# Optimization experiments

Measured on AMD Instinct MI355X. Metric: run time of the kernel, lower is better.

## Reference

```python
import jax, jax.numpy as jnp
import numpy as np

DIM = 64
NUM_GRAPHS = 512


def setup_inputs() -> dict:
    key = jax.random.key(0)
    ks = jax.random.split(key, 24)
    N, E, F = 20000, 60000, 11
    rn = lambda k, s, sc: jax.random.normal(k, s, jnp.float32) * sc
    return {
        "x": jax.random.normal(ks[0], (N, F), jnp.float32),
        "edge_index": jax.random.randint(ks[1], (2, E), 0, N),
        "edge_attr": jax.random.uniform(ks[2], (E, 5), jnp.float32),
        "batch": jnp.sort(jax.random.randint(ks[3], (N,), 0, NUM_GRAPHS)),
        # lin0: num_features -> dim
        "lin0_w": rn(ks[4], (DIM, F), 0.3), "lin0_b": jnp.zeros(DIM, jnp.float32),
        # edge MLP: 5 -> 128 -> dim*dim
        "nn1_w": rn(ks[5], (128, 5), 0.3), "nn1_b": jnp.zeros(128, jnp.float32),
        "nn2_w": rn(ks[6], (DIM * DIM, 128), 0.02), "nn2_b": jnp.zeros(DIM * DIM, jnp.float32),
        # NNConv root weight + bias
        "root_w": rn(ks[7], (DIM, DIM), 0.1), "conv_b": jnp.zeros(DIM, jnp.float32),
        # GRU (input dim, hidden dim) gates r,z,n
        "gru_w_ih": rn(ks[8], (3 * DIM, DIM), 0.1), "gru_w_hh": rn(ks[9], (3 * DIM, DIM), 0.1),
        "gru_b_ih": jnp.zeros(3 * DIM, jnp.float32), "gru_b_hh": jnp.zeros(3 * DIM, jnp.float32),
        # Set2Set LSTM: input 2*dim, hidden dim, gates i,f,g,o
        "lstm_w_ih": rn(ks[10], (4 * DIM, 2 * DIM), 0.1), "lstm_w_hh": rn(ks[11], (4 * DIM, DIM), 0.1),
        "lstm_b_ih": jnp.zeros(4 * DIM, jnp.float32), "lstm_b_hh": jnp.zeros(4 * DIM, jnp.float32),
        # readout
        "lin1_w": rn(ks[12], (DIM, 2 * DIM), 0.1), "lin1_b": jnp.zeros(DIM, jnp.float32),
        "lin2_w": rn(ks[13], (1, DIM), 0.1), "lin2_b": jnp.zeros(1, jnp.float32),
    }


def reference(x, edge_index, edge_attr, batch,
              lin0_w, lin0_b, nn1_w, nn1_b, nn2_w, nn2_b, root_w, conv_b,
              gru_w_ih, gru_w_hh, gru_b_ih, gru_b_hh,
              lstm_w_ih, lstm_w_hh, lstm_b_ih, lstm_b_hh,
              lin1_w, lin1_b, lin2_w, lin2_b):
    N = x.shape[0]
    src, dst = edge_index[0], edge_index[1]
    # per-edge weight matrices from edge MLP (edge_attr is constant across the 3 conv calls)
    We = (jax.nn.relu(edge_attr @ nn1_w.T + nn1_b) @ nn2_w.T + nn2_b).reshape(-1, DIM, DIM)
    deg = jnp.maximum(jax.ops.segment_sum(jnp.ones_like(src, jnp.float32), dst, N), 1.0)[:, None]

    out = jax.nn.relu(x @ lin0_w.T + lin0_b)
    h = out  # GRU hidden, shape [N, dim]
    for _ in range(3):
        # NNConv: gather src -> per-edge matmul -> scatter-mean at dst, plus root + bias
        msg = jnp.einsum('ei,eio->eo', out[src], We)
        agg = jax.ops.segment_sum(msg, dst, N) / deg
        m = jax.nn.relu(agg + out @ root_w.T + conv_b)
        # single GRU step (PyTorch gate layout r,z,n)
        gi = m @ gru_w_ih.T + gru_b_ih
        gh = h @ gru_w_hh.T + gru_b_hh
        ir, iz, inn = jnp.split(gi, 3, -1)
        hr, hz, hn = jnp.split(gh, 3, -1)
        r = jax.nn.sigmoid(ir + hr)
        z = jax.nn.sigmoid(iz + hz)
        n = jnp.tanh(inn + r * hn)
        h = (1.0 - z) * n + z * h
        out = h

    # Set2Set pooling, 3 processing steps
    B = NUM_GRAPHS
    q_star = jnp.zeros((B, 2 * DIM), out.dtype)
    hs = jnp.zeros((B, DIM), out.dtype)
    cs = jnp.zeros((B, DIM), out.dtype)
    for _ in range(3):
        gates = q_star @ lstm_w_ih.T + lstm_b_ih + hs @ lstm_w_hh.T + lstm_b_hh
        gi, gf, gg, go = jnp.split(gates, 4, -1)
        cs = jax.nn.sigmoid(gf) * cs + jax.nn.sigmoid(gi) * jnp.tanh(gg)
        hs = jax.nn.sigmoid(go) * jnp.tanh(cs)
        q = hs
        e = jnp.sum(out * q[batch], axis=-1)                 # [N]
        emax = jax.ops.segment_max(e, batch, B)
        a = jnp.exp(e - emax[batch])
        a = a / jax.ops.segment_sum(a, batch, B)[batch]      # scatter-softmax
        r_ = jax.ops.segment_sum(a[:, None] * out, batch, B)  # [B, dim]
        q_star = jnp.concatenate([q, r_], axis=-1)

    y = jax.nn.relu(q_star @ lin1_w.T + lin1_b) @ lin2_w.T + lin2_b
    return y.reshape(-1)
```

## Files before the change

kernel.cpp:

```cpp
#include <hip/hip_runtime.h>
#include <math.h>


typedef _Float16 f16x8 __attribute__((ext_vector_type(8)));
typedef _Float16 h2 __attribute__((ext_vector_type(2)));
typedef float f32x4 __attribute__((ext_vector_type(4)));

#define BFRAG_TOTAL (66 * 4 * 4 * 64 * 8)
#define PAIRS_CAP 40064
#define PMAX 152
#define SPLITK 4
#define ITERS 8

#if __has_builtin(__builtin_amdgcn_fdot2)
#define FDOT2(a, b, c) __builtin_amdgcn_fdot2((a), (b), (c), false)
#else
__device__ __forceinline__ float FDOT2(h2 a, h2 b, float c) {
  return c + (float)a[0] * (float)b[0] + (float)a[1] * (float)b[1];
}
#endif

__global__ void k_gptr(const int* __restrict__ batch, int* __restrict__ gptr,
                       int N, int B) {
  int n = blockIdx.x * 256 + threadIdx.x;
  if (n >= N) return;
  int b = batch[n];
  int bp = (n == 0) ? -1 : batch[n - 1];
  for (int g = bp + 1; g <= b; ++g) gptr[g] = n;
  if (n == N - 1) {
    for (int g = b + 1; g <= B; ++g) gptr[g] = N;
  }
}

__global__ void k_cnt(const int* __restrict__ eidx, int* __restrict__ cnt, int E) {
  int e = blockIdx.x * 256 + threadIdx.x;
  if (e < E) atomicAdd(&cnt[eidx[E + e]], 1);
}

__global__ __launch_bounds__(1024) void k_scan(const int* __restrict__ cnt,
                                               int* __restrict__ dptr2, int N) {
  __shared__ int wsum[16];
  int t = threadIdx.x;
  int lane = t & 63, wid = t >> 6;
  if (t == 0) dptr2[0] = 0;
  int running = 0;
  for (int base = 0; base < N; base += 1024) {
    int x = (base + t < N) ? ((cnt[base + t] + 1) & ~1) : 0;
#pragma unroll
    for (int d = 1; d < 64; d <<= 1) {
      int u = __shfl_up(x, d, 64);
      if (lane >= d) x += u;
    }
    if (lane == 63) wsum[wid] = x;
    __syncthreads();
    if (wid == 0) {
      int y = (lane < 16) ? wsum[lane] : 0;
#pragma unroll
      for (int d = 1; d < 16; d <<= 1) {
        int u = __shfl_up(y, d, 64);
        if (lane >= d) y += u;
      }
      if (lane < 16) wsum[lane] = y;
    }
    __syncthreads();
    int add = running + (wid > 0 ? wsum[wid - 1] : 0);
    if (base + t < N) dptr2[base + t + 1] = add + x;
    running += wsum[15];
    __syncthreads();
  }
}

__global__ void k_fill(const int* __restrict__ eidx, const int* __restrict__ dptr2,
                       int* __restrict__ fill, int* __restrict__ srcs_s,
                       int* __restrict__ eord, int E) {
  int e = blockIdx.x * 256 + threadIdx.x;
  if (e >= E) return;
  int d = eidx[E + e];
  int pos = dptr2[d] + atomicAdd(&fill[d], 1);
  srcs_s[pos] = eidx[e];
  eord[pos] = e;
}

__global__ __launch_bounds__(256) void k_h1t(const float* __restrict__ eattr,
                                             const int* __restrict__ eord,
                                             const int* __restrict__ eidx,
                                             const int* __restrict__ cnt,
                                             const float* __restrict__ nn1_w,
                                             const float* __restrict__ nn1_b,
                                             f16x8* __restrict__ hp, int E) {
  __shared__ float w5[640];
  __shared__ float bb[128];
  __shared__ float at[128][10];
  __shared__ float idg[128];
  __shared__ float vf1[128];
  const int t = threadIdx.x;
  const int m0 = blockIdx.x * 128;
  for (int idx = t; idx < 640; idx += 256) w5[idx] = nn1_w[idx];
  if (t < 128) bb[t] = nn1_b[t];
  if (t < 128) {
    int m = m0 + t;
    int e0 = eord[2 * m], e1 = eord[2 * m + 1];
    float iv = 0.f, vf = 0.f;
    if (e0 >= 0) {
      const float* a = eattr + (size_t)e0 * 5;
#pragma unroll
      for (int q = 0; q < 5; ++q) at[t][q] = a[q];
      int dg = cnt[eidx[E + e0]];
      iv = 1.f / (float)(dg > 1 ? dg : 1);
      if (e1 >= 0) {
        const float* b = eattr + (size_t)e1 * 5;
#pragma unroll
        for (int q = 0; q < 5; ++q) at[t][5 + q] = b[q];
        vf = 1.f;
      } else {
#pragma unroll
        for (int q = 0; q < 5; ++q) at[t][5 + q] = 0.f;
      }
    } else {
#pragma unroll
      for (int q = 0; q < 10; ++q) at[t][q] = 0.f;
    }
    idg[t] = iv;
    vf1[t] = vf;
  }
  __syncthreads();
  const int pl = t & 127, jh = (t >> 7) * 64;
  const int m = m0 + pl;
  float a0 = at[pl][0], a1 = at[pl][1], a2 = at[pl][2], a3 = at[pl][3],
        a4 = at[pl][4];
  float b0 = at[pl][5], b1 = at[pl][6], b2 = at[pl][7], b3 = at[pl][8],
        b4 = at[pl][9];
  float iv = idg[pl], vf = vf1[pl];
#pragma unroll 4
  for (int ci = 0; ci < 16; ++ci) {
    int j0 = jh + ci * 4;
    f16x8 o;
#pragma unroll
    for (int u = 0; u < 4; ++u) {
      const float* wr = &w5[(j0 + u) * 5];
      float v0 = fmaxf(bb[j0 + u] + a0 * wr[0] + a1 * wr[1] + a2 * wr[2] +
                           a3 * wr[3] + a4 * wr[4], 0.f) * iv;
      float v1 = fmaxf(bb[j0 + u] + b0 * wr[0] + b1 * wr[1] + b2 * wr[2] +
                           b3 * wr[3] + b4 * wr[4], 0.f) * iv * vf;
      o[2 * u] = (_Float16)v0;
      o[2 * u + 1] = (_Float16)v1;
    }
    hp[(size_t)(j0 >> 2) * PAIRS_CAP + m] = o;
  }
}

__global__ __launch_bounds__(256) void k_bsplit(
    const float* __restrict__ nn2_w, const float* __restrict__ nn2_b,
    const float* __restrict__ root_w, _Float16* __restrict__ Bh,
    _Float16* __restrict__ Bl) {
  __shared__ float lds[4096 * 2];
  const int kc = blockIdx.x;
  const int t = threadIdx.x;
  if (kc < 64) {
    for (int r = t; r < 4096; r += 256) {
      float2 v = *(const float2*)&nn2_w[(size_t)r * 128 + kc * 2];
      lds[r * 2] = v.x;
      lds[r * 2 + 1] = v.y;
    }
  } else if (kc == 64) {
    for (int r = t; r < 4096; r += 256) {
      lds[r * 2] = nn2_b[r];
      lds[r * 2 + 1] = 0.f;
    }
  } else {
    for (int r = t; r < 4096; r += 256) {
      int i = r >> 6, o = r & 63;
      lds[r * 2] = root_w[o * 64 + i];
      lds[r * 2 + 1] = 0.f;
    }
  }
  __syncthreads();
  for (int slot = t; slot < 1024; slot += 256) {
    int lane = slot & 63, c = (slot >> 6) & 3, w = slot >> 8;
    f16x8 ph, pl;
#pragma unroll
    for (int j = 0; j < 8; ++j) {
      int mm = w * 32 + ((lane >> 4) << 3) + j;
      int o = c * 16 + (lane & 15);
      int i = mm & 63, kl = mm >> 6;
      float v = lds[(i * 64 + o) * 2 + kl];
      _Float16 h = (_Float16)v;
      ph[j] = h;
      pl[j] = (_Float16)(v - (float)h);
    }
    size_t base = (((size_t)kc * 4 + w) * 4 + c) * 512 + (size_t)lane * 8;
    *(f16x8*)&Bh[base] = ph;
    *(f16x8*)&Bl[base] = pl;
  }
}

__global__ void k_lin0(const float* __restrict__ x, const float* __restrict__ w,
                       const float* __restrict__ b, float* __restrict__ outn, int N) {
  int gid = blockIdx.x * 256 + threadIdx.x;
  int n = gid >> 6, d = gid & 63;
  if (n >= N) return;
  const float* xr = x + (size_t)n * 11;
  const float* wr = w + d * 11;
  float acc = b[d];
#pragma unroll
  for (int f = 0; f < 11; ++f) acc += xr[f] * wr[f];
  outn[(size_t)n * 64 + d] = fmaxf(acc, 0.f);
}

__global__ __launch_bounds__(512, 4) void k_fused(
    const float* __restrict__ outn, const f16x8* __restrict__ hp,
    const int* __restrict__ dptr2, const int* __restrict__ cnt,
    const int* __restrict__ srcs_s, const _Float16* __restrict__ Bh,
    const _Float16* __restrict__ Bl, float* __restrict__ agg2, int N) {
  __shared__ __align__(16) _Float16 Ah[32 * 64 * 8];
  __shared__ uint4 sbufq[PMAX * 17];
  __shared__ uint4 hpq[2][PMAX];

  const int t = threadIdx.x;
  const int w = t >> 6, lane = t & 63;
  const int wq = w & 3;
  const int c_off = (w >> 2) * 2;
  const int nl = t >> 3;
  const int io = t & 7;
  const int split = blockIdx.y;
  const int n0 = blockIdx.x * 64;
  const int n = n0 + nl;
  const bool nvalid = (n < N);
  const int hi_n = (n0 + 64 > N) ? N : (n0 + 64);
  const int p0b = dptr2[n0];
  const int p1b = dptr2[hi_n];
  const int MP0 = p0b >> 1;
  const int MPn = (p1b - p0b) >> 1;
  const bool useLds = (MPn <= PMAX);
  int mp0 = 0, mp1 = 0, deg = 0;
  if (nvalid) { mp0 = dptr2[n] >> 1; mp1 = dptr2[n + 1] >> 1; deg = cnt[n]; }
  const float inv = 1.f / (float)(deg > 1 ? deg : 1);
  const int odd = deg & 1;
  const int rt_b = nl >> 4, nm = nl & 15;
  const int MPs = useLds ? MPn : 0;

  for (int idx = t; idx < MPs * 16; idx += 512) {
    int ml = idx >> 4, g = idx & 15;
    int e0s = srcs_s[2 * (MP0 + ml)];
    int e1s = srcs_s[2 * (MP0 + ml) + 1];
    float4 r0 = *(const float4*)(outn + (size_t)e0s * 64 + g * 4);
    float4 r1 = *(const float4*)(outn + (size_t)e1s * 64 + g * 4);
    f16x8 o;
    o[0] = (_Float16)r0.x; o[1] = (_Float16)r1.x;
    o[2] = (_Float16)r0.y; o[3] = (_Float16)r1.y;
    o[4] = (_Float16)r0.z; o[5] = (_Float16)r1.z;
    o[6] = (_Float16)r0.w; o[7] = (_Float16)r1.w;
    sbufq[ml * 17 + (((g >> 2) ^ (ml & 3)) << 2) + (g & 3)] =
        __builtin_bit_cast(uint4, o);
  }
  for (int idx = t; idx < MPs; idx += 512)
    hpq[0][idx] =
        *(const uint4*)&hp[(size_t)(split * ITERS) * PAIRS_CAP + MP0 + idx];
  __syncthreads();

  f32x4 acc[4][2];
#pragma unroll
  for (int a = 0; a < 4; ++a)
#pragma unroll
    for (int c = 0; c < 2; ++c) acc[a][c] = (f32x4)(0.f);

  const int niter = (split == 0) ? (ITERS + 1) : ITERS;
  int cur = 0;
  for (int cc = 0; cc < niter; ++cc) {
    const bool extra = (cc == ITERS);

    float av[4][8];
#pragma unroll
    for (int kl = 0; kl < 4; ++kl)
#pragma unroll
      for (int j = 0; j < 8; ++j) av[kl][j] = 0.f;

    if (!extra) {
      if (useLds) {
        for (int m = mp0; m < mp1; ++m) {
          int ml = m - MP0;
          uint4 hu = hpq[cur][ml];
          h2 h0 = __builtin_bit_cast(h2, hu.x);
          h2 h1 = __builtin_bit_cast(h2, hu.y);
          h2 hh2 = __builtin_bit_cast(h2, hu.z);
          h2 h3 = __builtin_bit_cast(h2, hu.w);
          int sb = ml * 17 + (((io >> 1) ^ (ml & 3)) << 2) + (io & 1) * 2;
          uint4 su0 = sbufq[sb], su1 = sbufq[sb + 1];
          unsigned vs[8] = {su0.x, su0.y, su0.z, su0.w,
                            su1.x, su1.y, su1.z, su1.w};
#pragma unroll
          for (int v = 0; v < 8; ++v) {
            h2 sp = __builtin_bit_cast(h2, vs[v]);
            av[0][v] = FDOT2(h0, sp, av[0][v]);
            av[1][v] = FDOT2(h1, sp, av[1][v]);
            av[2][v] = FDOT2(hh2, sp, av[2][v]);
            av[3][v] = FDOT2(h3, sp, av[3][v]);
          }
        }
      } else {
        const f16x8* hc = hp + (size_t)(split * ITERS + cc) * PAIRS_CAP;
        for (int m = mp0; m < mp1; ++m) {
          f16x8 hv = hc[m];
          int e0s = srcs_s[2 * m], e1s = srcs_s[2 * m + 1];
          const float4* pa = (const float4*)(outn + (size_t)e0s * 64 + io * 8);
          const float4* pb = (const float4*)(outn + (size_t)e1s * 64 + io * 8);
          float4 a0 = pa[0], a1 = pa[1];
          float4 c0 = pb[0], c1 = pb[1];
          float sv0[8] = {a0.x, a0.y, a0.z, a0.w, a1.x, a1.y, a1.z, a1.w};
          float sv1[8] = {c0.x, c0.y, c0.z, c0.w, c1.x, c1.y, c1.z, c1.w};
#pragma unroll
          for (int kl = 0; kl < 4; ++kl) {
            float hA = (float)hv[2 * kl], hB = (float)hv[2 * kl + 1];
#pragma unroll
            for (int j = 0; j < 8; ++j)
              av[kl][j] += hA * sv0[j] + hB * sv1[j];
          }
        }
      }
    } else {
      if (useLds) {
        for (int m = mp0; m < mp1; ++m) {
          int ml = m - MP0;
          h2 msk;
          msk[0] = (_Float16)1.f;
          msk[1] = (_Float16)((odd && m == mp1 - 1) ? 0.f : 1.f);
          int sb = ml * 17 + (((io >> 1) ^ (ml & 3)) << 2) + (io & 1) * 2;
          uint4 su0 = sbufq[sb], su1 = sbufq[sb + 1];
          unsigned vs[8] = {su0.x, su0.y, su0.z, su0.w,
                            su1.x, su1.y, su1.z, su1.w};
#pragma unroll
          for (int v = 0; v < 8; ++v) {
            h2 sp = __builtin_bit_cast(h2, vs[v]);
            av[0][v] = FDOT2(msk, sp, av[0][v]);
          }
        }
      } else {
        for (int m = mp0; m < mp1; ++m) {
          float m1 = (odd && m == mp1 - 1) ? 0.f : 1.f;
          int e0s = srcs_s[2 * m], e1s = srcs_s[2 * m + 1];
          const float4* pa = (const float4*)(outn + (size_t)e0s * 64 + io * 8);
          const float4* pb = (const float4*)(outn + (size_t)e1s * 64 + io * 8);
          float4 a0 = pa[0], a1 = pa[1];
          float4 c0 = pb[0], c1 = pb[1];
          float sv0[8] = {a0.x, a0.y, a0.z, a0.w, a1.x, a1.y, a1.z, a1.w};
          float sv1[8] = {c0.x, c0.y, c0.z, c0.w, c1.x, c1.y, c1.z, c1.w};
#pragma unroll
          for (int j = 0; j < 8; ++j) av[0][j] += sv0[j] + m1 * sv1[j];
        }
      }
#pragma unroll
      for (int j = 0; j < 8; ++j) av[0][j] *= inv;
      if (nvalid) {
        const float4* sp = (const float4*)(outn + (size_t)n * 64 + io * 8);
        float4 s0 = sp[0], s1 = sp[1];
        float sv[8] = {s0.x, s0.y, s0.z, s0.w, s1.x, s1.y, s1.z, s1.w};
#pragma unroll
        for (int j = 0; j < 8; ++j) av[2][j] = sv[j];
      }
    }

#pragma unroll
    for (int kl = 0; kl < 4; ++kl) {
      const int wb = (kl & 1) * 2 + (io >> 2);
      const int q = ((io >> 1) & 1) * 2 + (io & 1);
      const int fb = (kl >> 1) * 16 + wb * 4 + rt_b;
      const int base = (fb * 64 + (q << 4) + nm) * 8;
      f16x8 phv;
#pragma unroll
      for (int jj = 0; jj < 8; ++jj) phv[jj] = (_Float16)av[kl][jj];
      *(f16x8*)&Ah[base] = phv;
    }
    __syncthreads();

#pragma unroll
    for (int ph = 0; ph < 2; ++ph) {
      const int kco = extra ? (64 + ph) : (split * 16 + cc * 2 + ph);
      f16x8 ah[4];
#pragma unroll
      for (int rt = 0; rt < 4; ++rt)
        ah[rt] = *(const f16x8*)&Ah[((ph * 16 + wq * 4 + rt) * 64 + lane) * 8];
      if (ph == 0 && t < 256 && cc + 1 < ITERS) {
        const uint4* hc =
            (const uint4*)&hp[(size_t)(split * ITERS + cc + 1) * PAIRS_CAP + MP0];
        for (int idx = t; idx < MPs; idx += 256) hpq[cur ^ 1][idx] = hc[idx];
      }
      size_t bbase = ((size_t)(kco * 4 + wq) * 4) * 512;
#pragma unroll
      for (int c2 = 0; c2 < 2; ++c2) {
        const int c = c_off + c2;
        f16x8 bh = *(const f16x8*)&Bh[bbase + c * 512 + lane * 8];
        f16x8 bl = *(const f16x8*)&Bl[bbase + c * 512 + lane * 8];
#pragma unroll
        for (int rt = 0; rt < 4; ++rt) {
          acc[rt][c2] = __builtin_amdgcn_mfma_f32_16x16x32_f16(ah[rt], bh, acc[rt][c2], 0, 0, 0);
          acc[rt][c2] = __builtin_amdgcn_mfma_f32_16x16x32_f16(ah[rt], bl, acc[rt][c2], 0, 0, 0);
        }
      }
    }
    __syncthreads();
    if (cc + 1 < ITERS) cur ^= 1;
  }

  {
    float* redb = (float*)Ah;
    const int qrow = (lane >> 4) * 4, col15 = lane & 15;
    const int g14 = ((lane >> 4) & 1) << 4;
    if (wq == 1 || wq == 3) {
      float* L = redb + (wq >> 1) * 4096;
#pragma unroll
      for (int rt = 0; rt < 4; ++rt)
#pragma unroll
        for (int r = 0; r < 4; ++r) {
          int row = rt * 16 + qrow + r;
#pragma unroll
          for (int c2 = 0; c2 < 2; ++c2) {
            int col = (c_off + c2) * 16 + col15;
            L[row * 64 + (col ^ g14)] = acc[rt][c2][r];
          }
        }
    }
    __syncthreads();
    if (wq == 0 || wq == 2) {
      const float* L = redb + (wq >> 1) * 4096;
#pragma unroll
      for (int rt = 0; rt < 4; ++rt)
#pragma unroll
        for (int r = 0; r < 4; ++r) {
          int row = rt * 16 + qrow + r;
#pragma unroll
          for (int c2 = 0; c2 < 2; ++c2) {
            int col = (c_off + c2) * 16 + col15;
            acc[rt][c2][r] += L[row * 64 + (col ^ g14)];
          }
        }
    }
    __syncthreads();
    if (wq == 2) {
      float* L = redb;
#pragma unroll
      for (int rt = 0; rt < 4; ++rt)
#pragma unroll
        for (int r = 0; r < 4; ++r) {
          int row = rt * 16 + qrow + r;
#pragma unroll
          for (int c2 = 0; c2 < 2; ++c2) {
            int col = (c_off + c2) * 16 + col15;
            L[row * 64 + (col ^ g14)] = acc[rt][c2][r];
          }
        }
    }
    __syncthreads();
    if (wq == 0) {
      const float* L = redb;
      float* ag = agg2 + (size_t)split * (size_t)N * 64;
#pragma unroll
      for (int rt = 0; rt < 4; ++rt)
#pragma unroll
        for (int r = 0; r < 4; ++r) {
          int row = rt * 16 + qrow + r;
          int nn = n0 + row;
          if (nn < N) {
#pragma unroll
            for (int c2 = 0; c2 < 2; ++c2) {
              int col = (c_off + c2) * 16 + col15;
              float v = acc[rt][c2][r] + L[row * 64 + (col ^ g14)];
              ag[(size_t)nn * 64 + col] = v;
            }
          }
        }
    }
  }
}

__global__ __launch_bounds__(256) void k_gru(
    const float* __restrict__ agg2, const float* __restrict__ conv_b,
    const float* __restrict__ gw_ih, const float* __restrict__ gw_hh,
    const float* __restrict__ gb_ih, const float* __restrict__ gb_hh,
    float* __restrict__ outn, int N) {
  __shared__ float wT[32 * 385];
  const int t = threadIdx.x;
  const int wv = t >> 6, d = t & 63;
  const int nbase = blockIdx.x * 16 + wv * 4;
  const size_t NN = (size_t)N * 64;
  float m_d[4], h_d[4];
  bool act[4];
#pragma unroll
  for (int j = 0; j < 4; ++j) {
    int n = nbase + j;
    act[j] = (n < N);
    if (act[j]) {
      size_t idx = (size_t)n * 64 + d;
      float s = agg2[idx] + agg2[NN + idx] + agg2[2 * NN + idx] +
                agg2[3 * NN + idx];
      m_d[j] = fmaxf(s + conv_b[d], 0.f);
      h_d[j] = outn[idx];
    } else {
      m_d[j] = 0.f;
      h_d[j] = 0.f;
    }
  }
  float ir[4] = {0, 0, 0, 0}, iz[4] = {0, 0, 0, 0}, in_[4] = {0, 0, 0, 0};
  float hr[4] = {0, 0, 0, 0}, hz[4] = {0, 0, 0, 0}, hn[4] = {0, 0, 0, 0};
  for (int half = 0; half < 2; ++half) {
    __syncthreads();
    for (int idx = t; idx < 192 * 32; idx += 256) {
      int g = idx >> 5, kl = idx & 31;
      wT[kl * 385 + g] = gw_ih[g * 64 + half * 32 + kl];
      wT[kl * 385 + 192 + g] = gw_hh[g * 64 + half * 32 + kl];
    }
    __syncthreads();
#pragma unroll
    for (int kl = 0; kl < 32; ++kl) {
      int k = half * 32 + kl;
      const float* row = &wT[kl * 385];
      float r0 = row[d], r1 = row[64 + d], r2 = row[128 + d];
      float r3 = row[192 + d], r4 = row[256 + d], r5 = row[320 + d];
#pragma unroll
      for (int j = 0; j < 4; ++j) {
        float mk = __shfl(m_d[j], k);
        float hk = __shfl(h_d[j], k);
        ir[j] += r0 * mk;
        iz[j] += r1 * mk;
        in_[j] += r2 * mk;
        hr[j] += r3 * hk;
        hz[j] += r4 * hk;
        hn[j] += r5 * hk;
      }
    }
  }
#pragma unroll
  for (int j = 0; j < 4; ++j) {
    if (act[j]) {
      int n = nbase + j;
      float r = 1.f / (1.f + expf(-(ir[j] + gb_ih[d] + hr[j] + gb_hh[d])));
      float z = 1.f / (1.f + expf(-(iz[j] + gb_ih[64 + d] + hz[j] + gb_hh[64 + d])));
      float nn = tanhf(in_[j] + gb_ih[128 + d] + r * (hn[j] + gb_hh[128 + d]));
      outn[(size_t)n * 64 + d] = (1.f - z) * nn + z * h_d[j];
    }
  }
}

__global__ __launch_bounds__(256) void k_s2s(
    const float* __restrict__ outn, const int* __restrict__ gptr,
    const float* __restrict__ w_ih, const float* __restrict__ w_hh,
    const float* __restrict__ b_ih, const float* __restrict__ b_hh,
    const float* __restrict__ w1, const float* __restrict__ b1,
    const float* __restrict__ w2, const float* __restrict__ b2,
    float* __restrict__ y) {
  __shared__ float q[128];
  __shared__ float hsL[64];
  __shared__ float csL[64];
  __shared__ float gate[256];
  __shared__ float red[4][66];
  const int b = blockIdx.x, t = threadIdx.x;
  const int wv = t >> 6, d = t & 63;
  const int n0 = gptr[b], n1 = gptr[b + 1];
  if (t < 128) q[t] = 0.f;
  if (t < 64) { hsL[t] = 0.f; csL[t] = 0.f; }
  __syncthreads();

  for (int step = 0; step < 3; ++step) {
    float acc = b_ih[t] + b_hh[t];
    const float* wi = w_ih + t * 128;
    const float* wh = w_hh + t * 64;
#pragma unroll 4
    for (int k = 0; k < 128; ++k) acc += wi[k] * q[k];
#pragma unroll 4
    for (int k = 0; k < 64; ++k) acc += wh[k] * hsL[k];
    gate[t] = acc;
    __syncthreads();
    if (t < 64) {
      float ig = gate[t], fg = gate[64 + t], gg = gate[128 + t],
            og = gate[192 + t];
      float c = csL[t];
      float si = 1.f / (1.f + expf(-ig));
      float sf = 1.f / (1.f + expf(-fg));
      float so = 1.f / (1.f + expf(-og));
      float cn = sf * c + si * tanhf(gg);
      csL[t] = cn;
      hsL[t] = so * tanhf(cn);
    }
    __syncthreads();

    float qd = hsL[d];
    float mx = -3.4e38f, den = 0.f, racc = 0.f;
    for (int nn = n0 + wv; nn < n1; nn += 4) {
      float od = outn[(size_t)nn * 64 + d];
      float v = od * qd;
      for (int s = 32; s > 0; s >>= 1) v += __shfl_xor(v, s);
      float mnew = fmaxf(mx, v);
      float scale = expf(mx - mnew);
      float a = expf(v - mnew);
      den = den * scale + a;
      racc = racc * scale + a * od;
      mx = mnew;
    }
    if (d == 0) { red[wv][0] = mx; red[wv][1] = den; }
    red[wv][2 + d] = racc;
    __syncthreads();
    if (t < 64) {
      float M = fmaxf(fmaxf(red[0][0], red[1][0]), fmaxf(red[2][0], red[3][0]));
      float dd = 0.f, rr = 0.f;
#pragma unroll
      for (int ww = 0; ww < 4; ++ww) {
        float sc = expf(red[ww][0] - M);
        dd += red[ww][1] * sc;
        rr += red[ww][2 + t] * sc;
      }
      float r = (dd > 0.f) ? rr / dd : 0.f;
      q[t] = hsL[t];
      q[64 + t] = r;
    }
    __syncthreads();
  }

  if (t < 64) {
    float acc = b1[t];
    const float* wr = w1 + t * 128;
#pragma unroll 4
    for (int k = 0; k < 128; ++k) acc += wr[k] * q[k];
    acc = fmaxf(acc, 0.f) * w2[t];
    for (int s = 32; s > 0; s >>= 1) acc += __shfl_xor(acc, s);
    if (t == 0) y[b] = acc + b2[0];
  }
}

extern "C" void kernel_launch(void* const* d_in, const int* in_sizes, int n_in,
                              void* d_out, int out_size, void* d_ws,
                              size_t ws_size, hipStream_t stream) {
  (void)n_in; (void)out_size; (void)ws_size;
  const float* x      = (const float*)d_in[0];
  const int*   eidx   = (const int*)d_in[1];
  const float* eattr  = (const float*)d_in[2];
  const int*   batch  = (const int*)d_in[3];
  const float* lin0_w = (const float*)d_in[4];
  const float* lin0_b = (const float*)d_in[5];
  const float* nn1_w  = (const float*)d_in[6];
  const float* nn1_b  = (const float*)d_in[7];
  const float* nn2_w  = (const float*)d_in[8];
  const float* nn2_b  = (const float*)d_in[9];
  const float* root_w = (const float*)d_in[10];
  const float* conv_b = (const float*)d_in[11];
  const float* gw_ih  = (const float*)d_in[12];
  const float* gw_hh  = (const float*)d_in[13];
  const float* gb_ih  = (const float*)d_in[14];
  const float* gb_hh  = (const float*)d_in[15];
  const float* lw_ih  = (const float*)d_in[16];
  const float* lw_hh  = (const float*)d_in[17];
  const float* lb_ih  = (const float*)d_in[18];
  const float* lb_hh  = (const float*)d_in[19];
  const float* lin1_w = (const float*)d_in[20];
  const float* lin1_b = (const float*)d_in[21];
  const float* lin2_w = (const float*)d_in[22];
  const float* lin2_b = (const float*)d_in[23];

  const int N = in_sizes[0] / 11;
  const int E = in_sizes[1] / 2;
  const int B = 512;

  size_t off = 0;
  auto bump = [&](size_t bytes) {
    size_t o = off;
    off += (bytes + 255) & ~(size_t)255;
    return o;
  };
  char* base = (char*)d_ws;
  float*     outn   = (float*)(base + bump((size_t)N * 64 * 4));
  float*     agg2   = (float*)(base + bump((size_t)SPLITK * N * 64 * 4));
  f16x8*     hpG    = (f16x8*)(base + bump((size_t)32 * PAIRS_CAP * 16));
  _Float16*  Bh     = (_Float16*)(base + bump((size_t)BFRAG_TOTAL * 2));
  _Float16*  Bl     = (_Float16*)(base + bump((size_t)BFRAG_TOTAL * 2));
  int*       cnt    = (int*)(base + bump((size_t)2 * N * 4));
  int*       fill   = cnt + N;
  int*       dptr2  = (int*)(base + bump((size_t)(N + 1) * 4));
  int*       srcs_s = (int*)(base + bump((size_t)2 * PAIRS_CAP * 4));
  int*       eord   = (int*)(base + bump((size_t)2 * PAIRS_CAP * 4));
  int*       gptr   = (int*)(base + bump((size_t)(B + 1) * 4));

  hipMemsetAsync(cnt, 0, (size_t)2 * N * 4, stream);
  hipMemsetAsync(srcs_s, 0, (size_t)2 * PAIRS_CAP * 4, stream);
  hipMemsetAsync(eord, 0xFF, (size_t)2 * PAIRS_CAP * 4, stream);

  k_gptr<<<(N + 255) / 256, 256, 0, stream>>>(batch, gptr, N, B);
  k_cnt<<<(E + 255) / 256, 256, 0, stream>>>(eidx, cnt, E);
  k_scan<<<1, 1024, 0, stream>>>(cnt, dptr2, N);
  k_fill<<<(E + 255) / 256, 256, 0, stream>>>(eidx, dptr2, fill, srcs_s, eord, E);
  k_h1t<<<PAIRS_CAP / 128, 256, 0, stream>>>(eattr, eord, eidx, cnt, nn1_w,
                                             nn1_b, hpG, E);
  k_bsplit<<<66, 256, 0, stream>>>(nn2_w, nn2_b, root_w, Bh, Bl);
  k_lin0<<<(N * 64 + 255) / 256, 256, 0, stream>>>(x, lin0_w, lin0_b, outn, N);

  const int NBLK = (N + 63) / 64;
  for (int it = 0; it < 3; ++it) {
    k_fused<<<dim3(NBLK, SPLITK), 512, 0, stream>>>(outn, hpG, dptr2, cnt,
                                                    srcs_s, Bh, Bl, agg2, N);
    k_gru<<<(N + 15) / 16, 256, 0, stream>>>(agg2, conv_b, gw_ih, gw_hh, gb_ih,
                                             gb_hh, outn, N);
  }

  k_s2s<<<B, 256, 0, stream>>>(outn, gptr, lw_ih, lw_hh, lb_ih, lb_hh, lin1_w,
                               lin1_b, lin2_w, lin2_b, (float*)d_out);
}
```

Before: 715.9 us.

## Move GRU gate matmuls onto MFMA with split-fp16 pre-packed weights

Replaces the scalar FMA/shuffle GRU kernel with one that stages the [m|h] activations as fp16 A-fragments in LDS. It computes the r, z and n gate products with 16x16x32 f16 MFMAs against weights pre-split into high and low fp16 halves by a new one-time packing kernel. The goal is to cut the FP32 ALU cost and the per-block weight transpose into LDS that each GRU launch repeated. In exchange, activations are rounded to a single fp16, which loses precision, and the bias and gate math now sit in the MFMA output layout.

```diff
diff --git a/kernel.cpp b/kernel.cpp
--- a/kernel.cpp
+++ b/kernel.cpp
@@ -7,6 +7,7 @@
 typedef float f32x4 __attribute__((ext_vector_type(4)));
 
 #define BFRAG_TOTAL (66 * 4 * 4 * 64 * 8)
+#define GFRAG_TOTAL (4 * 16 * 64 * 8)
 #define PAIRS_CAP 40064
 #define PMAX 152
 #define SPLITK 4
@@ -194,6 +195,38 @@
   }
 }
 
+__global__ __launch_bounds__(256) void k_gsplit(
+    const float* __restrict__ gw_ih, const float* __restrict__ gw_hh,
+    _Float16* __restrict__ Gh, _Float16* __restrict__ Gl) {
+  const int c = blockIdx.x;
+  const int t = threadIdx.x;
+  const int w = t >> 6, lane = t & 63;
+  const int part = c >> 2, dblk = c & 3;
+  f16x8 oh, ol;
+#pragma unroll
+  for (int j = 0; j < 8; ++j) {
+    int k = w * 32 + ((lane >> 4) << 3) + j;
+    int d = dblk * 16 + (lane & 15);
+    float v;
+    if (part == 0) {
+      v = (k < 64) ? gw_ih[(size_t)d * 64 + k] : gw_hh[(size_t)d * 64 + (k - 64)];
+    } else if (part == 1) {
+      v = (k < 64) ? gw_ih[(size_t)(64 + d) * 64 + k]
+                   : gw_hh[(size_t)(64 + d) * 64 + (k - 64)];
+    } else if (part == 2) {
+      v = (k < 64) ? gw_ih[(size_t)(128 + d) * 64 + k] : 0.f;
+    } else {
+      v = (k >= 64) ? gw_hh[(size_t)(128 + d) * 64 + (k - 64)] : 0.f;
+    }
+    _Float16 h = (_Float16)v;
+    oh[j] = h;
+    ol[j] = (_Float16)(v - (float)h);
+  }
+  size_t base = ((size_t)(w * 16 + c) * 64 + lane) * 8;
+  *(f16x8*)&Gh[base] = oh;
+  *(f16x8*)&Gl[base] = ol;
+}
+
 __global__ void k_lin0(const float* __restrict__ x, const float* __restrict__ w,
                        const float* __restrict__ b, float* __restrict__ outn, int N) {
   int gid = blockIdx.x * 256 + threadIdx.x;
@@ -472,70 +505,99 @@
   }
 }
 
-__global__ __launch_bounds__(256) void k_gru(
+__global__ __launch_bounds__(512) void k_gru2(
     const float* __restrict__ agg2, const float* __restrict__ conv_b,
-    const float* __restrict__ gw_ih, const float* __restrict__ gw_hh,
+    const _Float16* __restrict__ Gh, const _Float16* __restrict__ Gl,
     const float* __restrict__ gb_ih, const float* __restrict__ gb_hh,
     float* __restrict__ outn, int N) {
-  __shared__ float wT[32 * 385];
+  __shared__ __align__(16) _Float16 Afrag[16 * 64 * 8];
+  __shared__ float bih[192], bhh[192];
   const int t = threadIdx.x;
-  const int wv = t >> 6, d = t & 63;
-  const int nbase = blockIdx.x * 16 + wv * 4;
+  const int n0 = blockIdx.x * 64;
   const size_t NN = (size_t)N * 64;
-  float m_d[4], h_d[4];
-  bool act[4];
-#pragma unroll
-  for (int j = 0; j < 4; ++j) {
-    int n = nbase + j;
-    act[j] = (n < N);
-    if (act[j]) {
-      size_t idx = (size_t)n * 64 + d;
-      float s = agg2[idx] + agg2[NN + idx] + agg2[2 * NN + idx] +
-                agg2[3 * NN + idx];
-      m_d[j] = fmaxf(s + conv_b[d], 0.f);
-      h_d[j] = outn[idx];
+  if (t < 192) { bih[t] = gb_ih[t]; bhh[t] = gb_hh[t]; }
+
+  {
+    const int nl = t >> 3, io = t & 7;
+    const int n = n0 + nl;
+    float v[16];
+    if (n < N) {
+      if (io < 4) {
+        const int d0 = io * 16;
+        const size_t base = (size_t)n * 64 + d0;
+#pragma unroll
+        for (int q = 0; q < 4; ++q) {
+          float4 s0 = *(const float4*)&agg2[base + q * 4];
+          float4 s1 = *(const float4*)&agg2[NN + base + q * 4];
+          float4 s2 = *(const float4*)&agg2[2 * NN + base + q * 4];
+          float4 s3 = *(const float4*)&agg2[3 * NN + base + q * 4];
+          float4 cb = *(const float4*)&conv_b[d0 + q * 4];
+          v[q * 4 + 0] = fmaxf(s0.x + s1.x + s2.x + s3.x + cb.x, 0.f);
+          v[q * 4 + 1] = fmaxf(s0.y + s1.y + s2.y + s3.y + cb.y, 0.f);
+          v[q * 4 + 2] = fmaxf(s0.z + s1.z + s2.z + s3.z + cb.z, 0.f);
+          v[q * 4 + 3] = fmaxf(s0.w + s1.w + s2.w + s3.w + cb.w, 0.f);
+        }
+      } else {
+        const int d0 = (io - 4) * 16;
+#pragma unroll
+        for (int q = 0; q < 4; ++q) {
+          float4 h4 = *(const float4*)&outn[(size_t)n * 64 + d0 + q * 4];
+          v[q * 4 + 0] = h4.x;
+          v[q * 4 + 1] = h4.y;
+          v[q * 4 + 2] = h4.z;
+          v[q * 4 + 3] = h4.w;
+        }
+      }
     } else {
-      m_d[j] = 0.f;
-      h_d[j] = 0.f;
-    }
-  }
-  float ir[4] = {0, 0, 0, 0}, iz[4] = {0, 0, 0, 0}, in_[4] = {0, 0, 0, 0};
-  float hr[4] = {0, 0, 0, 0}, hz[4] = {0, 0, 0, 0}, hn[4] = {0, 0, 0, 0};
-  for (int half = 0; half < 2; ++half) {
-    __syncthreads();
-    for (int idx = t; idx < 192 * 32; idx += 256) {
-      int g = idx >> 5, kl = idx & 31;
-      wT[kl * 385 + g] = gw_ih[g * 64 + half * 32 + kl];
-      wT[kl * 385 + 192 + g] = gw_hh[g * 64 + half * 32 + kl];
-    }
-    __syncthreads();
-#pragma unroll
-    for (int kl = 0; kl < 32; ++kl) {
-      int k = half * 32 + kl;
-      const float* row = &wT[kl * 385];
-      float r0 = row[d], r1 = row[64 + d], r2 = row[128 + d];
-      float r3 = row[192 + d], r4 = row[256 + d], r5 = row[320 + d];
-#pragma unroll
-      for (int j = 0; j < 4; ++j) {
-        float mk = __shfl(m_d[j], k);
-        float hk = __shfl(h_d[j], k);
-        ir[j] += r0 * mk;
-        iz[j] += r1 * mk;
-        in_[j] += r2 * mk;
-        hr[j] += r3 * hk;
-        hz[j] += r4 * hk;
-        hn[j] += r5 * hk;
-      }
-    }
-  }
-#pragma unroll
-  for (int j = 0; j < 4; ++j) {
-    if (act[j]) {
-      int n = nbase + j;
-      float r = 1.f / (1.f + expf(-(ir[j] + gb_ih[d] + hr[j] + gb_hh[d])));
-      float z = 1.f / (1.f + expf(-(iz[j] + gb_ih[64 + d] + hz[j] + gb_hh[64 + d])));
-      float nn = tanhf(in_[j] + gb_ih[128 + d] + r * (hn[j] + gb_hh[128 + d]));
-      outn[(size_t)n * 64 + d] = (1.f - z) * nn + z * h_d[j];
+#pragma unroll
+      for (int j = 0; j < 16; ++j) v[j] = 0.f;
+    }
+    const int rt = nl >> 4, m = nl & 15;
+#pragma unroll
+    for (int g2 = 0; g2 < 2; ++g2) {
+      int k0 = io * 16 + g2 * 8;
+      int ksub = k0 >> 5, kgrp = (k0 >> 3) & 3;
+      f16x8 o;
+#pragma unroll
+      for (int jj = 0; jj < 8; ++jj) o[jj] = (_Float16)v[g2 * 8 + jj];
+      *(f16x8*)&Afrag[((ksub * 4 + rt) * 64 + (kgrp << 4) + m) * 8] = o;
+    }
+  }
+  __syncthreads();
+
+  const int w = t >> 6, lane = t & 63;
+  const int rt = w >> 1, q2 = (w & 1) * 2;
+  f32x4 acc[8];
+#pragma unroll
+  for (int i = 0; i < 8; ++i) acc[i] = (f32x4)(0.f);
+#pragma unroll
+  for (int ks = 0; ks < 4; ++ks) {
+    f16x8 ah = *(const f16x8*)&Afrag[((ks * 4 + rt) * 64 + lane) * 8];
+#pragma unroll
+    for (int idx = 0; idx < 8; ++idx) {
+      int c = (idx >> 1) * 4 + q2 + (idx & 1);
+      f16x8 gh = *(const f16x8*)&Gh[((size_t)(ks * 16 + c) * 64 + lane) * 8];
+      f16x8 gl = *(const f16x8*)&Gl[((size_t)(ks * 16 + c) * 64 + lane) * 8];
+      acc[idx] = __builtin_amdgcn_mfma_f32_16x16x32_f16(ah, gh, acc[idx], 0, 0, 0);
+      acc[idx] = __builtin_amdgcn_mfma_f32_16x16x32_f16(ah, gl, acc[idx], 0, 0, 0);
+    }
+  }
+  const int qrow = (lane >> 4) * 4, col = lane & 15;
+#pragma unroll
+  for (int c01 = 0; c01 < 2; ++c01) {
+    const int d = (q2 + c01) * 16 + col;
+#pragma unroll
+    for (int r = 0; r < 4; ++r) {
+      const int n = n0 + rt * 16 + qrow + r;
+      if (n < N) {
+        float rs = acc[c01][r], zs = acc[2 + c01][r];
+        float inn = acc[4 + c01][r], hn = acc[6 + c01][r];
+        float h = outn[(size_t)n * 64 + d];
+        float rg = 1.f / (1.f + expf(-(rs + bih[d] + bhh[d])));
+        float zg = 1.f / (1.f + expf(-(zs + bih[64 + d] + bhh[64 + d])));
+        float ng = tanhf(inn + bih[128 + d] + rg * (hn + bhh[128 + d]));
+        outn[(size_t)n * 64 + d] = (1.f - zg) * ng + zg * h;
+      }
     }
   }
 }
@@ -670,6 +732,8 @@
   f16x8*     hpG    = (f16x8*)(base + bump((size_t)32 * PAIRS_CAP * 16));
   _Float16*  Bh     = (_Float16*)(base + bump((size_t)BFRAG_TOTAL * 2));
   _Float16*  Bl     = (_Float16*)(base + bump((size_t)BFRAG_TOTAL * 2));
+  _Float16*  Gh     = (_Float16*)(base + bump((size_t)GFRAG_TOTAL * 2));
+  _Float16*  Gl     = (_Float16*)(base + bump((size_t)GFRAG_TOTAL * 2));
   int*       cnt    = (int*)(base + bump((size_t)2 * N * 4));
   int*       fill   = cnt + N;
   int*       dptr2  = (int*)(base + bump((size_t)(N + 1) * 4));
@@ -688,14 +752,15 @@
   k_h1t<<<PAIRS_CAP / 128, 256, 0, stream>>>(eattr, eord, eidx, cnt, nn1_w,
                                              nn1_b, hpG, E);
   k_bsplit<<<66, 256, 0, stream>>>(nn2_w, nn2_b, root_w, Bh, Bl);
+  k_gsplit<<<16, 256, 0, stream>>>(gw_ih, gw_hh, Gh, Gl);
   k_lin0<<<(N * 64 + 255) / 256, 256, 0, stream>>>(x, lin0_w, lin0_b, outn, N);
 
   const int NBLK = (N + 63) / 64;
   for (int it = 0; it < 3; ++it) {
     k_fused<<<dim3(NBLK, SPLITK), 512, 0, stream>>>(outn, hpG, dptr2, cnt,
                                                     srcs_s, Bh, Bl, agg2, N);
-    k_gru<<<(N + 15) / 16, 256, 0, stream>>>(agg2, conv_b, gw_ih, gw_hh, gb_ih,
-                                             gb_hh, outn, N);
+    k_gru2<<<NBLK, 512, 0, stream>>>(agg2, conv_b, Gh, Gl, gb_ih, gb_hh, outn,
+                                     N);
   }
 
   k_s2s<<<B, 256, 0, stream>>>(outn, gptr, lw_ih, lw_hh, lb_ih, lb_hh, lin1_w,
```

Measured after the change: 628.8 us. 12.2% less time.
